# Kernel tuning notes

Measured on AMD Instinct MI355X. Metric: run time of the kernel, lower is better.

Reference implementation:

```python
import jax, jax.numpy as jnp
import numpy as np

IMG = 640
STRIDES = (8, 16, 32)
NUM_CLASSES = 80
TOPK = 10
A_ALPHA = 0.5
A_BETA = 6.0
EPS = 1e-7
CLS_W = 1.0
BOX_W = 2.5


def _make_anchors():
    anchors, strides = [], []
    for s in STRIDES:
        n = IMG // s
        gy, gx = np.meshgrid(np.arange(n, dtype=np.float32), np.arange(n, dtype=np.float32), indexing='ij')
        anchors.append(np.stack([(gx.ravel() + 0.5) * s, (gy.ravel() + 0.5) * s], -1))
        strides.append(np.full((n * n,), s, dtype=np.float32))
    return jnp.asarray(np.concatenate(anchors, 0)), jnp.asarray(np.concatenate(strides, 0))


def _cxcywh_to_xyxy(b):
    cx, cy, w, h = b[..., 0], b[..., 1], b[..., 2], b[..., 3]
    return jnp.stack([cx - w / 2, cy - h / 2, cx + w / 2, cy + h / 2], -1)


def _decode(pred_boxes, anchors, strides):
    # pred_boxes: (B, A, 4) ltrb distances; anchors (A,2); strides (A,)
    d = jax.nn.relu(pred_boxes) * strides[None, :, None]
    x1 = anchors[None, :, 0] - d[..., 0]
    y1 = anchors[None, :, 1] - d[..., 1]
    x2 = anchors[None, :, 0] + d[..., 2]
    y2 = anchors[None, :, 1] + d[..., 3]
    return jnp.stack([x1, y1, x2, y2], -1)


def _box_iou_vs_gt(boxes, gt):
    # boxes: (B, A, 4) xyxy, gt: (B, 4) xyxy -> (B, A)
    lt = jnp.maximum(boxes[..., :2], gt[:, None, :2])
    rb = jnp.minimum(boxes[..., 2:], gt[:, None, 2:])
    wh = jnp.clip(rb - lt, 0.0)
    inter = wh[..., 0] * wh[..., 1]
    a1 = (boxes[..., 2] - boxes[..., 0]) * (boxes[..., 3] - boxes[..., 1])
    a2 = (gt[:, 2] - gt[:, 0]) * (gt[:, 3] - gt[:, 1])
    return inter / (a1 + a2[:, None] - inter)


def _assign(pred_scores, pred_bboxes, anchors, gt_labels, gt_xyxy):
    # Vectorized TaskAlignedAssigner for exactly one gt box per image.
    B, A, C = pred_scores.shape
    cx, cy = anchors[:, 0][None], anchors[:, 1][None]  # (1, A)
    gx1, gy1, gx2, gy2 = (gt_xyxy[:, i:i + 1] for i in range(4))  # (B, 1)
    gt_valid = ((gx2 > gx1) & (gy2 > gy1))[:, 0]  # (B,)
    inside = (cx >= gx1) & (cx <= gx2) & (cy >= gy1) & (cy <= gy2)  # (B, A)
    dist = (cx - (gx1 + gx2) / 2) ** 2 + (cy - (gy1 + gy2) / 2) ** 2
    fallback = jax.nn.one_hot(jnp.argmin(dist, 1), A, dtype=bool)  # nearest anchor if none inside
    mask = jnp.where(inside.any(1, keepdims=True), inside, fallback)
    ious = jnp.clip(_box_iou_vs_gt(pred_bboxes, gt_xyxy), 1e-9)
    cls_s = jax.nn.sigmoid(jnp.take_along_axis(pred_scores, gt_labels[:, None, None], 2)[..., 0])  # (B, A)
    metric = jnp.where(mask, cls_s ** A_ALPHA * ious ** A_BETA, -jnp.inf)
    top_m, top_i = jax.lax.top_k(metric, TOPK)  # (B, TOPK)
    keep = jnp.isfinite(top_m) & gt_valid[:, None]  # handles variable k = min(topk, n_valid) and degenerate gts
    bidx = jnp.arange(B)[:, None]
    fg = jnp.zeros((B, A), bool).at[bidx, top_i].max(keep)
    top_iou = jnp.take_along_axis(ious, top_i, 1)
    tscores = jnp.zeros((B, A, C), pred_scores.dtype).at[bidx, top_i, gt_labels[:, None]].max(jnp.where(keep, top_iou, 0.0))
    tboxes = jnp.where(fg[..., None], gt_xyxy[:, None, :], 0.0)
    return tboxes, tscores, fg


def _focal_sum(logits, targets, alpha=0.25, gamma=2.0):
    p = jax.nn.sigmoid(logits)
    ce = jnp.maximum(logits, 0.0) - logits * targets + jnp.log1p(jnp.exp(-jnp.abs(logits)))
    pt = p * targets + (1 - p) * (1 - targets)
    at = alpha * targets + (1 - alpha) * (1 - targets)
    return jnp.sum(at * ce * (1 - pt) ** gamma)


def _ciou(b1, b2):
    b1x1, b1y1, b1x2, b1y2 = b1[..., 0], b1[..., 1], b1[..., 2], b1[..., 3]
    b2x1, b2y1, b2x2, b2y2 = b2[..., 0], b2[..., 1], b2[..., 2], b2[..., 3]
    w1, h1 = b1x2 - b1x1, b1y2 - b1y1
    w2, h2 = b2x2 - b2x1, b2y2 - b2y1
    inter = jnp.clip(jnp.minimum(b1x2, b2x2) - jnp.maximum(b1x1, b2x1), 0.0) * jnp.clip(jnp.minimum(b1y2, b2y2) - jnp.maximum(b1y1, b2y1), 0.0)
    union = w1 * h1 + w2 * h2 - inter + EPS
    iou = inter / union
    cw = jnp.maximum(b1x2, b2x2) - jnp.minimum(b1x1, b2x1)
    ch = jnp.maximum(b1y2, b2y2) - jnp.minimum(b1y1, b2y1)
    c2 = cw ** 2 + ch ** 2 + EPS
    rho2 = ((b2x1 + b2x2 - b1x1 - b1x2) ** 2 + (b2y1 + b2y2 - b1y1 - b1y2) ** 2) / 4
    v = (4 / jnp.pi ** 2) * (jnp.arctan(w2 / (h2 + EPS)) - jnp.arctan(w1 / (h1 + EPS))) ** 2
    alpha = jax.lax.stop_gradient(v / (v - iou + (1 + EPS)))
    return 1 - iou + rho2 / c2 + alpha * v


def _loss(pred_boxes, pred_scores, gt_bboxes, gt_labels):
    anchors, strides = _make_anchors()
    gt_xyxy = _cxcywh_to_xyxy(gt_bboxes)  # (B, 4)
    pred_xyxy = _decode(pred_boxes, anchors, strides)  # (B, A, 4)
    tboxes, tscores, fg = jax.lax.stop_gradient(
        _assign(pred_scores, pred_xyxy, anchors, gt_labels, gt_xyxy))
    loss_cls = _focal_sum(pred_scores, tscores)
    # mask instead of boolean-index: use pred box as dummy target where not fg (loss masked to 0)
    safe_t = jax.lax.stop_gradient(jnp.where(fg[..., None], tboxes, pred_xyxy))
    loss_box = jnp.sum(_ciou(pred_xyxy, safe_t) * fg.astype(pred_xyxy.dtype))
    npos = jnp.maximum(fg.sum().astype(pred_scores.dtype), 1.0)
    return (loss_cls / npos) * CLS_W + (loss_box / npos) * BOX_W


def setup_inputs() -> dict:
    key = jax.random.key(0)
    k1, k2, k3, k4, k5 = jax.random.split(key, 5)
    B, A, C = 64, 8400, NUM_CLASSES
    pred_boxes = jax.random.normal(k1, (B, A, 4), jnp.float32) + 1.0
    pred_scores = jax.random.normal(k2, (B, A, C), jnp.float32)
    cxcy = jax.random.uniform(k3, (B, 2), jnp.float32, 120.0, 520.0)
    wh = jax.random.uniform(k4, (B, 2), jnp.float32, 60.0, 220.0)
    gt_bboxes = jnp.concatenate([cxcy, wh], -1)  # valid cxcywh boxes inside 640x640
    gt_labels = jax.random.randint(k5, (B,), 0, C)
    return {"pred_boxes": pred_boxes, "pred_scores": pred_scores, "gt_bboxes": gt_bboxes, "gt_labels": gt_labels}


def reference(pred_boxes, pred_scores, gt_bboxes, gt_labels):
    return _loss(pred_boxes, pred_scores, gt_bboxes, gt_labels)
```

## Files before the change

kernel.cpp:

```cpp
#include <hip/hip_runtime.h>
#include <math.h>

#define NCLS 80
#define A_TOT 8400
#define TOPK 10
#define NB_A 64
#define NB_F 448
#define BLK 1024
#define CAND_CAP 1536


__device__ __forceinline__ void anchor_of(int a, float& cx, float& cy, float& st) {
    if (a < 6400)      { int r = a / 80;          int c = a - r * 80;          cx = (c + 0.5f) * 8.0f;  cy = (r + 0.5f) * 8.0f;  st = 8.0f;  }
    else if (a < 8000) { int i = a - 6400; int r = i / 40; int c = i - r * 40; cx = (c + 0.5f) * 16.0f; cy = (r + 0.5f) * 16.0f; st = 16.0f; }
    else               { int i = a - 8000; int r = i / 20; int c = i - r * 20; cx = (c + 0.5f) * 32.0f; cy = (r + 0.5f) * 32.0f; st = 32.0f; }
}

__device__ __forceinline__ float focal0(float l) {
    float e  = __expf(-fabsf(l));
    float ce = fmaxf(l, 0.0f) + __logf(1.0f + e);
    float r  = 1.0f / (1.0f + e);
    float p  = (l >= 0.0f) ? r : e * r;
    return 0.75f * ce * p * p;
}

__device__ __forceinline__ float focal_t(float l, float t) {
    float e  = __expf(-fabsf(l));
    float ce = fmaxf(l, 0.0f) - l * t + __logf(1.0f + e);
    float r  = 1.0f / (1.0f + e);
    float p  = (l >= 0.0f) ? r : e * r;
    float pt = p * t + (1.0f - p) * (1.0f - t);
    float at = 0.75f - 0.5f * t;
    float om = 1.0f - pt;
    return at * ce * om * om;
}

__device__ __forceinline__ float ciou_(float b1x1, float b1y1, float b1x2, float b1y2,
                                       float b2x1, float b2y1, float b2x2, float b2y2) {
    const float EPS = 1e-7f;
    float w1 = b1x2 - b1x1, h1 = b1y2 - b1y1;
    float w2 = b2x2 - b2x1, h2 = b2y2 - b2y1;
    float iw = fmaxf(fminf(b1x2, b2x2) - fmaxf(b1x1, b2x1), 0.0f);
    float ih = fmaxf(fminf(b1y2, b2y2) - fmaxf(b1y1, b2y1), 0.0f);
    float inter = iw * ih;
    float uni = w1 * h1 + w2 * h2 - inter + EPS;
    float iou = inter / uni;
    float cw = fmaxf(b1x2, b2x2) - fminf(b1x1, b2x1);
    float ch = fmaxf(b1y2, b2y2) - fminf(b1y1, b2y1);
    float c2 = cw * cw + ch * ch + EPS;
    float dx = b2x1 + b2x2 - b1x1 - b1x2;
    float dy = b2y1 + b2y2 - b1y1 - b1y2;
    float rho2 = (dx * dx + dy * dy) * 0.25f;
    const float k = 4.0f / (float)(M_PI * M_PI);
    float dv = atanf(w2 / (h2 + EPS)) - atanf(w1 / (h1 + EPS));
    float v = k * dv * dv;
    float alpha = v / (v - iou + 1.0f + EPS);
    return 1.0f - iou + rho2 / c2 + alpha * v;
}


__global__ __launch_bounds__(BLK) void fused_kernel(const float* __restrict__ pred_boxes,
                                                    const float* __restrict__ pred_scores,
                                                    const float* __restrict__ gt_bboxes,
                                                    const int* __restrict__ gt_labels,
                                                    float* __restrict__ ws_focal,
                                                    float* __restrict__ ws_corr,
                                                    float* __restrict__ ws_box,
                                                    int*   __restrict__ ws_np,
                                                    int n4) {
    const int tid = threadIdx.x;

    __shared__ float s_rv[16];
    __shared__ int   s_ri[16];

    if (blockIdx.x >= NB_A) {
        const int fb = blockIdx.x - NB_A;
        float acc = 0.0f;
        const float4* p = (const float4*)pred_scores;
        for (int i = fb * BLK + tid; i < n4; i += NB_F * BLK) {
            float4 v = p[i];
            acc += focal0(v.x) + focal0(v.y) + focal0(v.z) + focal0(v.w);
        }
        for (int o = 32; o > 0; o >>= 1) acc += __shfl_down(acc, o, 64);
        if ((tid & 63) == 0) s_rv[tid >> 6] = acc;
        __syncthreads();
        if (tid < 16) {
            float v = s_rv[tid];
            for (int o = 8; o > 0; o >>= 1) v += __shfl_down(v, o, 64);
            if (tid == 0) ws_focal[fb] = v;
        }
        return;
    }

    const int b = blockIdx.x;

    __shared__ int   s_cnt;
    __shared__ float s_cm[CAND_CAP];
    __shared__ int   s_ci[CAND_CAP];
    __shared__ int   t_idx[TOPK];
    __shared__ float t_val[TOPK];
    __shared__ float s_corr[TOPK], s_boxl[TOPK];
    __shared__ int   s_keep[TOPK];

    const float gcx = gt_bboxes[b * 4 + 0], gcy = gt_bboxes[b * 4 + 1];
    const float gw  = gt_bboxes[b * 4 + 2], gh  = gt_bboxes[b * 4 + 3];
    const float gx1 = gcx - 0.5f * gw, gy1 = gcy - 0.5f * gh;
    const float gx2 = gcx + 0.5f * gw, gy2 = gcy + 0.5f * gh;
    const int   lb  = gt_labels[b];
    const bool  gt_valid = (gx2 > gx1) && (gy2 > gy1);
    const float garea = (gx2 - gx1) * (gy2 - gy1);
    const float gmx = 0.5f * (gx1 + gx2), gmy = 0.5f * (gy1 + gy2);

    if (tid == 0) s_cnt = 0;
    __syncthreads();

    float bestd = INFINITY;
    int   besti = 0x7fffffff;

    for (int a = tid; a < A_TOT; a += BLK) {
        float cx, cy, st;
        anchor_of(a, cx, cy, st);
        float4 pb = ((const float4*)pred_boxes)[b * A_TOT + a];
        float x1 = cx - fmaxf(pb.x, 0.0f) * st;
        float y1 = cy - fmaxf(pb.y, 0.0f) * st;
        float x2 = cx + fmaxf(pb.z, 0.0f) * st;
        float y2 = cy + fmaxf(pb.w, 0.0f) * st;
        bool inside = (cx >= gx1) && (cx <= gx2) && (cy >= gy1) && (cy <= gy2);
        if (inside) {
            float iw = fmaxf(fminf(x2, gx2) - fmaxf(x1, gx1), 0.0f);
            float ih = fmaxf(fminf(y2, gy2) - fmaxf(y1, gy1), 0.0f);
            float inter = iw * ih;
            float iou = fmaxf(inter / ((x2 - x1) * (y2 - y1) + garea - inter), 1e-9f);
            float sc = pred_scores[(size_t)(b * A_TOT + a) * NCLS + lb];
            float cls_s = 1.0f / (1.0f + __expf(-sc));
            float i2 = iou * iou;
            float m = sqrtf(cls_s) * i2 * i2 * i2;
            int pos = atomicAdd(&s_cnt, 1);
            if (pos < CAND_CAP) { s_cm[pos] = m; s_ci[pos] = a; }
        }
        float ddx = cx - gmx, ddy = cy - gmy;
        float d = ddx * ddx + ddy * ddy;
        if (d < bestd) { bestd = d; besti = a; }
    }
    __syncthreads();
    int cnt = min(s_cnt, CAND_CAP);

    if (cnt == 0) {
        float v = bestd; int i = besti;
        for (int o = 32; o > 0; o >>= 1) {
            float ov = __shfl_down(v, o, 64); int oi = __shfl_down(i, o, 64);
            if (ov < v || (ov == v && oi < i)) { v = ov; i = oi; }
        }
        if ((tid & 63) == 0) { s_rv[tid >> 6] = v; s_ri[tid >> 6] = i; }
        __syncthreads();
        if (tid < 16) {
            v = s_rv[tid]; i = s_ri[tid];
            for (int o = 8; o > 0; o >>= 1) {
                float ov = __shfl_down(v, o, 64); int oi = __shfl_down(i, o, 64);
                if (ov < v || (ov == v && oi < i)) { v = ov; i = oi; }
            }
            if (tid == 0) {
                int a = i;
                float cx, cy, st;
                anchor_of(a, cx, cy, st);
                float4 pb = ((const float4*)pred_boxes)[b * A_TOT + a];
                float x1 = cx - fmaxf(pb.x, 0.0f) * st;
                float y1 = cy - fmaxf(pb.y, 0.0f) * st;
                float x2 = cx + fmaxf(pb.z, 0.0f) * st;
                float y2 = cy + fmaxf(pb.w, 0.0f) * st;
                float iw = fmaxf(fminf(x2, gx2) - fmaxf(x1, gx1), 0.0f);
                float ih = fmaxf(fminf(y2, gy2) - fmaxf(y1, gy1), 0.0f);
                float inter = iw * ih;
                float iou = fmaxf(inter / ((x2 - x1) * (y2 - y1) + garea - inter), 1e-9f);
                float sc = pred_scores[(size_t)(b * A_TOT + a) * NCLS + lb];
                float cls_s = 1.0f / (1.0f + __expf(-sc));
                float i2 = iou * iou;
                s_cm[0] = sqrtf(cls_s) * i2 * i2 * i2;
                s_ci[0] = a;
            }
        }
        __syncthreads();
        cnt = 1;
    }

    for (int k = 0; k < TOPK; k++) {
        float v = -INFINITY; int i = 0x7fffffff;
        for (int p = tid; p < cnt; p += BLK) {
            float m = s_cm[p]; int a = s_ci[p];
            if (m > v || (m == v && a < i)) { v = m; i = a; }
        }
        for (int o = 32; o > 0; o >>= 1) {
            float ov = __shfl_down(v, o, 64); int oi = __shfl_down(i, o, 64);
            if (ov > v || (ov == v && oi < i)) { v = ov; i = oi; }
        }
        if ((tid & 63) == 0) { s_rv[tid >> 6] = v; s_ri[tid >> 6] = i; }
        __syncthreads();
        if (tid < 16) {
            v = s_rv[tid]; i = s_ri[tid];
            for (int o = 8; o > 0; o >>= 1) {
                float ov = __shfl_down(v, o, 64); int oi = __shfl_down(i, o, 64);
                if (ov > v || (ov == v && oi < i)) { v = ov; i = oi; }
            }
            if (tid == 0) { t_val[k] = v; t_idx[k] = i; }
        }
        __syncthreads();
        int wa = t_idx[k];
        if (t_val[k] > -INFINITY) {
            for (int p = tid; p < cnt; p += BLK)
                if (s_ci[p] == wa) s_cm[p] = -INFINITY;
        }
        __syncthreads();
    }

    if (tid < TOPK) {
        int   a = t_idx[tid];
        float v = t_val[tid];
        int keep = (v > -INFINITY) && gt_valid;
        float corr = 0.0f, boxl = 0.0f;
        if (keep) {
            float cx, cy, st;
            anchor_of(a, cx, cy, st);
            float4 pb = ((const float4*)pred_boxes)[b * A_TOT + a];
            float x1 = cx - fmaxf(pb.x, 0.0f) * st;
            float y1 = cy - fmaxf(pb.y, 0.0f) * st;
            float x2 = cx + fmaxf(pb.z, 0.0f) * st;
            float y2 = cy + fmaxf(pb.w, 0.0f) * st;
            float iw = fmaxf(fminf(x2, gx2) - fmaxf(x1, gx1), 0.0f);
            float ih = fmaxf(fminf(y2, gy2) - fmaxf(y1, gy1), 0.0f);
            float inter = iw * ih;
            float t = fmaxf(inter / ((x2 - x1) * (y2 - y1) + garea - inter), 1e-9f);
            float l = pred_scores[(size_t)(b * A_TOT + a) * NCLS + lb];
            corr = focal_t(l, t) - focal0(l);
            boxl = ciou_(x1, y1, x2, y2, gx1, gy1, gx2, gy2);
        }
        s_corr[tid] = corr;
        s_boxl[tid] = boxl;
        s_keep[tid] = keep;
    }
    __syncthreads();
    if (tid == 0) {
        float cs = 0.0f, bs = 0.0f;
        int np = 0;
        for (int k = 0; k < TOPK; k++) { cs += s_corr[k]; bs += s_boxl[k]; np += s_keep[k]; }
        ws_corr[b] = cs;
        ws_box[b]  = bs;
        ws_np[b]   = np;
    }
}


__global__ __launch_bounds__(64) void finalize_kernel(const float* __restrict__ ws_focal,
                                                      const float* __restrict__ ws_corr,
                                                      const float* __restrict__ ws_box,
                                                      const int* __restrict__ ws_np,
                                                      float* __restrict__ out, int B) {
    int tid = threadIdx.x;
    float c = 0.0f, bx = 0.0f;
    int np = 0;
    for (int i = tid; i < NB_F; i += 64) c += ws_focal[i];
    for (int i = tid; i < B; i += 64) { c += ws_corr[i]; bx += ws_box[i]; np += ws_np[i]; }
    for (int o = 32; o > 0; o >>= 1) {
        c  += __shfl_down(c, o, 64);
        bx += __shfl_down(bx, o, 64);
        np += __shfl_down(np, o, 64);
    }
    if (tid == 0) {
        float npos = fmaxf((float)np, 1.0f);
        out[0] = c / npos + 2.5f * bx / npos;
    }
}


extern "C" void kernel_launch(void* const* d_in, const int* in_sizes, int n_in,
                              void* d_out, int out_size, void* d_ws, size_t ws_size,
                              hipStream_t stream) {
    const float* pred_boxes  = (const float*)d_in[0];
    const float* pred_scores = (const float*)d_in[1];
    const float* gt_bboxes   = (const float*)d_in[2];
    const int*   gt_labels   = (const int*)d_in[3];
    float* out = (float*)d_out;

    const int B  = in_sizes[3];
    const int n4 = in_sizes[1] / 4;

    float* ws_focal = (float*)d_ws;
    float* ws_corr  = ws_focal + NB_F;
    float* ws_box   = ws_corr + B;
    int*   ws_np    = (int*)(ws_box + B);

    fused_kernel<<<NB_A + NB_F, BLK, 0, stream>>>(pred_boxes, pred_scores, gt_bboxes, gt_labels,
                                                  ws_focal, ws_corr, ws_box, ws_np, n4);
    finalize_kernel<<<1, 64, 0, stream>>>(ws_focal, ws_corr, ws_box, ws_np, out, B);
}
```

Measured before the change: 251.4 us.

## Use dynamic chunk scheduling for focal pass and fuse finalize via last-block reduction

All 512 blocks now take part in the dense focal sum, which pulls chunks of pred_scores from a global atomic counter. The 64 assignment blocks join the pool once their per-image top-k work finishes, so that work is balanced against the bandwidth-bound streaming. The separate finalize kernel is replaced by a last-block-done reduction inside the fused kernel, with workspace entries padded to cache lines. A small init kernel is added to reset the counters, and the chunk loop adds an atomic plus extra barriers per chunk.

After: 278.6 us. 10.8% more time.

```diff
diff --git a/kernel.cpp b/kernel.cpp
--- a/kernel.cpp
+++ b/kernel.cpp
@@ -5,9 +5,12 @@
 #define A_TOT 8400
 #define TOPK 10
 #define NB_A 64
-#define NB_F 448
+#define NBLK 512
 #define BLK 1024
 #define CAND_CAP 1536
+#define FITER 4
+#define CHUNK (BLK * FITER)
+#define LINE 32
 
 
 __device__ __forceinline__ void anchor_of(int a, float& cx, float& cy, float& st) {
@@ -59,41 +62,26 @@
 }
 
 
+__global__ __launch_bounds__(64) void init_kernel(int* __restrict__ counters) {
+    if (threadIdx.x < 2) counters[threadIdx.x] = 0;
+}
+
+
 __global__ __launch_bounds__(BLK) void fused_kernel(const float* __restrict__ pred_boxes,
                                                     const float* __restrict__ pred_scores,
                                                     const float* __restrict__ gt_bboxes,
                                                     const int* __restrict__ gt_labels,
+                                                    int*   __restrict__ counters,
                                                     float* __restrict__ ws_focal,
-                                                    float* __restrict__ ws_corr,
-                                                    float* __restrict__ ws_box,
-                                                    int*   __restrict__ ws_np,
-                                                    int n4) {
+                                                    float* __restrict__ ws_img,
+                                                    float* __restrict__ out,
+                                                    int n4, int B) {
     const int tid = threadIdx.x;
 
     __shared__ float s_rv[16];
     __shared__ int   s_ri[16];
-
-    if (blockIdx.x >= NB_A) {
-        const int fb = blockIdx.x - NB_A;
-        float acc = 0.0f;
-        const float4* p = (const float4*)pred_scores;
-        for (int i = fb * BLK + tid; i < n4; i += NB_F * BLK) {
-            float4 v = p[i];
-            acc += focal0(v.x) + focal0(v.y) + focal0(v.z) + focal0(v.w);
-        }
-        for (int o = 32; o > 0; o >>= 1) acc += __shfl_down(acc, o, 64);
-        if ((tid & 63) == 0) s_rv[tid >> 6] = acc;
-        __syncthreads();
-        if (tid < 16) {
-            float v = s_rv[tid];
-            for (int o = 8; o > 0; o >>= 1) v += __shfl_down(v, o, 64);
-            if (tid == 0) ws_focal[fb] = v;
-        }
-        return;
-    }
-
-    const int b = blockIdx.x;
-
+    __shared__ int   s_chunk;
+    __shared__ int   s_last;
     __shared__ int   s_cnt;
     __shared__ float s_cm[CAND_CAP];
     __shared__ int   s_ci[CAND_CAP];
@@ -102,65 +90,125 @@
     __shared__ float s_corr[TOPK], s_boxl[TOPK];
     __shared__ int   s_keep[TOPK];
 
-    const float gcx = gt_bboxes[b * 4 + 0], gcy = gt_bboxes[b * 4 + 1];
-    const float gw  = gt_bboxes[b * 4 + 2], gh  = gt_bboxes[b * 4 + 3];
-    const float gx1 = gcx - 0.5f * gw, gy1 = gcy - 0.5f * gh;
-    const float gx2 = gcx + 0.5f * gw, gy2 = gcy + 0.5f * gh;
-    const int   lb  = gt_labels[b];
-    const bool  gt_valid = (gx2 > gx1) && (gy2 > gy1);
-    const float garea = (gx2 - gx1) * (gy2 - gy1);
-    const float gmx = 0.5f * (gx1 + gx2), gmy = 0.5f * (gy1 + gy2);
-
-    if (tid == 0) s_cnt = 0;
-    __syncthreads();
-
-    float bestd = INFINITY;
-    int   besti = 0x7fffffff;
-
-    for (int a = tid; a < A_TOT; a += BLK) {
-        float cx, cy, st;
-        anchor_of(a, cx, cy, st);
-        float4 pb = ((const float4*)pred_boxes)[b * A_TOT + a];
-        float x1 = cx - fmaxf(pb.x, 0.0f) * st;
-        float y1 = cy - fmaxf(pb.y, 0.0f) * st;
-        float x2 = cx + fmaxf(pb.z, 0.0f) * st;
-        float y2 = cy + fmaxf(pb.w, 0.0f) * st;
-        bool inside = (cx >= gx1) && (cx <= gx2) && (cy >= gy1) && (cy <= gy2);
-        if (inside) {
-            float iw = fmaxf(fminf(x2, gx2) - fmaxf(x1, gx1), 0.0f);
-            float ih = fmaxf(fminf(y2, gy2) - fmaxf(y1, gy1), 0.0f);
-            float inter = iw * ih;
-            float iou = fmaxf(inter / ((x2 - x1) * (y2 - y1) + garea - inter), 1e-9f);
-            float sc = pred_scores[(size_t)(b * A_TOT + a) * NCLS + lb];
-            float cls_s = 1.0f / (1.0f + __expf(-sc));
-            float i2 = iou * iou;
-            float m = sqrtf(cls_s) * i2 * i2 * i2;
-            int pos = atomicAdd(&s_cnt, 1);
-            if (pos < CAND_CAP) { s_cm[pos] = m; s_ci[pos] = a; }
-        }
-        float ddx = cx - gmx, ddy = cy - gmy;
-        float d = ddx * ddx + ddy * ddy;
-        if (d < bestd) { bestd = d; besti = a; }
-    }
-    __syncthreads();
-    int cnt = min(s_cnt, CAND_CAP);
-
-    if (cnt == 0) {
-        float v = bestd; int i = besti;
-        for (int o = 32; o > 0; o >>= 1) {
-            float ov = __shfl_down(v, o, 64); int oi = __shfl_down(i, o, 64);
-            if (ov < v || (ov == v && oi < i)) { v = ov; i = oi; }
-        }
-        if ((tid & 63) == 0) { s_rv[tid >> 6] = v; s_ri[tid >> 6] = i; }
-        __syncthreads();
-        if (tid < 16) {
-            v = s_rv[tid]; i = s_ri[tid];
-            for (int o = 8; o > 0; o >>= 1) {
+    if (blockIdx.x < NB_A) {
+        const int b = blockIdx.x;
+
+        const float gcx = gt_bboxes[b * 4 + 0], gcy = gt_bboxes[b * 4 + 1];
+        const float gw  = gt_bboxes[b * 4 + 2], gh  = gt_bboxes[b * 4 + 3];
+        const float gx1 = gcx - 0.5f * gw, gy1 = gcy - 0.5f * gh;
+        const float gx2 = gcx + 0.5f * gw, gy2 = gcy + 0.5f * gh;
+        const int   lb  = gt_labels[b];
+        const bool  gt_valid = (gx2 > gx1) && (gy2 > gy1);
+        const float garea = (gx2 - gx1) * (gy2 - gy1);
+        const float gmx = 0.5f * (gx1 + gx2), gmy = 0.5f * (gy1 + gy2);
+
+        if (tid == 0) s_cnt = 0;
+        __syncthreads();
+
+        float bestd = INFINITY;
+        int   besti = 0x7fffffff;
+
+        for (int a = tid; a < A_TOT; a += BLK) {
+            float cx, cy, st;
+            anchor_of(a, cx, cy, st);
+            float4 pb = ((const float4*)pred_boxes)[b * A_TOT + a];
+            float x1 = cx - fmaxf(pb.x, 0.0f) * st;
+            float y1 = cy - fmaxf(pb.y, 0.0f) * st;
+            float x2 = cx + fmaxf(pb.z, 0.0f) * st;
+            float y2 = cy + fmaxf(pb.w, 0.0f) * st;
+            bool inside = (cx >= gx1) && (cx <= gx2) && (cy >= gy1) && (cy <= gy2);
+            if (inside) {
+                float iw = fmaxf(fminf(x2, gx2) - fmaxf(x1, gx1), 0.0f);
+                float ih = fmaxf(fminf(y2, gy2) - fmaxf(y1, gy1), 0.0f);
+                float inter = iw * ih;
+                float iou = fmaxf(inter / ((x2 - x1) * (y2 - y1) + garea - inter), 1e-9f);
+                float sc = pred_scores[(size_t)(b * A_TOT + a) * NCLS + lb];
+                float cls_s = 1.0f / (1.0f + __expf(-sc));
+                float i2 = iou * iou;
+                float m = sqrtf(cls_s) * i2 * i2 * i2;
+                int pos = atomicAdd(&s_cnt, 1);
+                if (pos < CAND_CAP) { s_cm[pos] = m; s_ci[pos] = a; }
+            }
+            float ddx = cx - gmx, ddy = cy - gmy;
+            float d = ddx * ddx + ddy * ddy;
+            if (d < bestd) { bestd = d; besti = a; }
+        }
+        __syncthreads();
+        int cnt = min(s_cnt, CAND_CAP);
+
+        if (cnt == 0) {
+            float v = bestd; int i = besti;
+            for (int o = 32; o > 0; o >>= 1) {
                 float ov = __shfl_down(v, o, 64); int oi = __shfl_down(i, o, 64);
                 if (ov < v || (ov == v && oi < i)) { v = ov; i = oi; }
             }
-            if (tid == 0) {
-                int a = i;
+            if ((tid & 63) == 0) { s_rv[tid >> 6] = v; s_ri[tid >> 6] = i; }
+            __syncthreads();
+            if (tid < 16) {
+                v = s_rv[tid]; i = s_ri[tid];
+                for (int o = 8; o > 0; o >>= 1) {
+                    float ov = __shfl_down(v, o, 64); int oi = __shfl_down(i, o, 64);
+                    if (ov < v || (ov == v && oi < i)) { v = ov; i = oi; }
+                }
+                if (tid == 0) {
+                    int a = i;
+                    float cx, cy, st;
+                    anchor_of(a, cx, cy, st);
+                    float4 pb = ((const float4*)pred_boxes)[b * A_TOT + a];
+                    float x1 = cx - fmaxf(pb.x, 0.0f) * st;
+                    float y1 = cy - fmaxf(pb.y, 0.0f) * st;
+                    float x2 = cx + fmaxf(pb.z, 0.0f) * st;
+                    float y2 = cy + fmaxf(pb.w, 0.0f) * st;
+                    float iw = fmaxf(fminf(x2, gx2) - fmaxf(x1, gx1), 0.0f);
+                    float ih = fmaxf(fminf(y2, gy2) - fmaxf(y1, gy1), 0.0f);
+                    float inter = iw * ih;
+                    float iou = fmaxf(inter / ((x2 - x1) * (y2 - y1) + garea - inter), 1e-9f);
+                    float sc = pred_scores[(size_t)(b * A_TOT + a) * NCLS + lb];
+                    float cls_s = 1.0f / (1.0f + __expf(-sc));
+                    float i2 = iou * iou;
+                    s_cm[0] = sqrtf(cls_s) * i2 * i2 * i2;
+                    s_ci[0] = a;
+                }
+            }
+            __syncthreads();
+            cnt = 1;
+        }
+
+        for (int k = 0; k < TOPK; k++) {
+            float v = -INFINITY; int i = 0x7fffffff;
+            for (int p = tid; p < cnt; p += BLK) {
+                float m = s_cm[p]; int a = s_ci[p];
+                if (m > v || (m == v && a < i)) { v = m; i = a; }
+            }
+            for (int o = 32; o > 0; o >>= 1) {
+                float ov = __shfl_down(v, o, 64); int oi = __shfl_down(i, o, 64);
+                if (ov > v || (ov == v && oi < i)) { v = ov; i = oi; }
+            }
+            if ((tid & 63) == 0) { s_rv[tid >> 6] = v; s_ri[tid >> 6] = i; }
+            __syncthreads();
+            if (tid < 16) {
+                v = s_rv[tid]; i = s_ri[tid];
+                for (int o = 8; o > 0; o >>= 1) {
+                    float ov = __shfl_down(v, o, 64); int oi = __shfl_down(i, o, 64);
+                    if (ov > v || (ov == v && oi < i)) { v = ov; i = oi; }
+                }
+                if (tid == 0) { t_val[k] = v; t_idx[k] = i; }
+            }
+            __syncthreads();
+            int wa = t_idx[k];
+            if (t_val[k] > -INFINITY) {
+                for (int p = tid; p < cnt; p += BLK)
+                    if (s_ci[p] == wa) s_cm[p] = -INFINITY;
+            }
+            __syncthreads();
+        }
+
+        if (tid < TOPK) {
+            int   a = t_idx[tid];
+            float v = t_val[tid];
+            int keep = (v > -INFINITY) && gt_valid;
+            float corr = 0.0f, boxl = 0.0f;
+            if (keep) {
                 float cx, cy, st;
                 anchor_of(a, cx, cy, st);
                 float4 pb = ((const float4*)pred_boxes)[b * A_TOT + a];
@@ -171,102 +219,81 @@
                 float iw = fmaxf(fminf(x2, gx2) - fmaxf(x1, gx1), 0.0f);
                 float ih = fmaxf(fminf(y2, gy2) - fmaxf(y1, gy1), 0.0f);
                 float inter = iw * ih;
-                float iou = fmaxf(inter / ((x2 - x1) * (y2 - y1) + garea - inter), 1e-9f);
-                float sc = pred_scores[(size_t)(b * A_TOT + a) * NCLS + lb];
-                float cls_s = 1.0f / (1.0f + __expf(-sc));
-                float i2 = iou * iou;
-                s_cm[0] = sqrtf(cls_s) * i2 * i2 * i2;
-                s_ci[0] = a;
-            }
-        }
-        __syncthreads();
-        cnt = 1;
+                float t = fmaxf(inter / ((x2 - x1) * (y2 - y1) + garea - inter), 1e-9f);
+                float l = pred_scores[(size_t)(b * A_TOT + a) * NCLS + lb];
+                corr = focal_t(l, t) - focal0(l);
+                boxl = ciou_(x1, y1, x2, y2, gx1, gy1, gx2, gy2);
+            }
+            s_corr[tid] = corr;
+            s_boxl[tid] = boxl;
+            s_keep[tid] = keep;
+        }
+        __syncthreads();
+        if (tid == 0) {
+            float cs = 0.0f, bs = 0.0f;
+            int np = 0;
+            for (int k = 0; k < TOPK; k++) { cs += s_corr[k]; bs += s_boxl[k]; np += s_keep[k]; }
+            float* L = ws_img + b * LINE;
+            L[0] = cs;
+            L[1] = bs;
+            L[2] = (float)np;
+        }
     }
 
-    for (int k = 0; k < TOPK; k++) {
-        float v = -INFINITY; int i = 0x7fffffff;
-        for (int p = tid; p < cnt; p += BLK) {
-            float m = s_cm[p]; int a = s_ci[p];
-            if (m > v || (m == v && a < i)) { v = m; i = a; }
-        }
-        for (int o = 32; o > 0; o >>= 1) {
-            float ov = __shfl_down(v, o, 64); int oi = __shfl_down(i, o, 64);
-            if (ov > v || (ov == v && oi < i)) { v = ov; i = oi; }
-        }
-        if ((tid & 63) == 0) { s_rv[tid >> 6] = v; s_ri[tid >> 6] = i; }
-        __syncthreads();
-        if (tid < 16) {
-            v = s_rv[tid]; i = s_ri[tid];
-            for (int o = 8; o > 0; o >>= 1) {
-                float ov = __shfl_down(v, o, 64); int oi = __shfl_down(i, o, 64);
-                if (ov > v || (ov == v && oi < i)) { v = ov; i = oi; }
-            }
-            if (tid == 0) { t_val[k] = v; t_idx[k] = i; }
-        }
-        __syncthreads();
-        int wa = t_idx[k];
-        if (t_val[k] > -INFINITY) {
-            for (int p = tid; p < cnt; p += BLK)
-                if (s_ci[p] == wa) s_cm[p] = -INFINITY;
-        }
-        __syncthreads();
+    float acc = 0.0f;
+    const float4* p4 = (const float4*)pred_scores;
+    if (tid == 0) s_chunk = atomicAdd(&counters[0], 1);
+    for (;;) {
+        __syncthreads();
+        const int c = s_chunk;
+        const int base = c * CHUNK;
+        if (base >= n4) break;
+        __syncthreads();
+        if (tid == 0) s_chunk = atomicAdd(&counters[0], 1);
+        #pragma unroll
+        for (int k = 0; k < FITER; k++) {
+            int i = base + k * BLK + tid;
+            if (i < n4) {
+                float4 v = p4[i];
+                acc += focal0(v.x) + focal0(v.y) + focal0(v.z) + focal0(v.w);
+            }
+        }
     }
 
-    if (tid < TOPK) {
-        int   a = t_idx[tid];
-        float v = t_val[tid];
-        int keep = (v > -INFINITY) && gt_valid;
-        float corr = 0.0f, boxl = 0.0f;
-        if (keep) {
-            float cx, cy, st;
-            anchor_of(a, cx, cy, st);
-            float4 pb = ((const float4*)pred_boxes)[b * A_TOT + a];
-            float x1 = cx - fmaxf(pb.x, 0.0f) * st;
-            float y1 = cy - fmaxf(pb.y, 0.0f) * st;
-            float x2 = cx + fmaxf(pb.z, 0.0f) * st;
-            float y2 = cy + fmaxf(pb.w, 0.0f) * st;
-            float iw = fmaxf(fminf(x2, gx2) - fmaxf(x1, gx1), 0.0f);
-            float ih = fmaxf(fminf(y2, gy2) - fmaxf(y1, gy1), 0.0f);
-            float inter = iw * ih;
-            float t = fmaxf(inter / ((x2 - x1) * (y2 - y1) + garea - inter), 1e-9f);
-            float l = pred_scores[(size_t)(b * A_TOT + a) * NCLS + lb];
-            corr = focal_t(l, t) - focal0(l);
-            boxl = ciou_(x1, y1, x2, y2, gx1, gy1, gx2, gy2);
-        }
-        s_corr[tid] = corr;
-        s_boxl[tid] = boxl;
-        s_keep[tid] = keep;
+    for (int o = 32; o > 0; o >>= 1) acc += __shfl_down(acc, o, 64);
+    if ((tid & 63) == 0) s_rv[tid >> 6] = acc;
+    __syncthreads();
+    if (tid == 0) {
+        float v = 0.0f;
+        #pragma unroll
+        for (int w = 0; w < BLK / 64; w++) v += s_rv[w];
+        ws_focal[blockIdx.x * LINE] = v;
+        __threadfence();
+        int old = atomicAdd(&counters[1], 1);
+        s_last = (old == NBLK - 1);
     }
     __syncthreads();
-    if (tid == 0) {
-        float cs = 0.0f, bs = 0.0f;
-        int np = 0;
-        for (int k = 0; k < TOPK; k++) { cs += s_corr[k]; bs += s_boxl[k]; np += s_keep[k]; }
-        ws_corr[b] = cs;
-        ws_box[b]  = bs;
-        ws_np[b]   = np;
-    }
-}
-
-
-__global__ __launch_bounds__(64) void finalize_kernel(const float* __restrict__ ws_focal,
-                                                      const float* __restrict__ ws_corr,
-                                                      const float* __restrict__ ws_box,
-                                                      const int* __restrict__ ws_np,
-                                                      float* __restrict__ out, int B) {
-    int tid = threadIdx.x;
-    float c = 0.0f, bx = 0.0f;
-    int np = 0;
-    for (int i = tid; i < NB_F; i += 64) c += ws_focal[i];
-    for (int i = tid; i < B; i += 64) { c += ws_corr[i]; bx += ws_box[i]; np += ws_np[i]; }
-    for (int o = 32; o > 0; o >>= 1) {
-        c  += __shfl_down(c, o, 64);
-        bx += __shfl_down(bx, o, 64);
-        np += __shfl_down(np, o, 64);
-    }
-    if (tid == 0) {
-        float npos = fmaxf((float)np, 1.0f);
-        out[0] = c / npos + 2.5f * bx / npos;
+
+    if (s_last) {
+        __threadfence();
+        if (tid < 64) {
+            float c = 0.0f, bx = 0.0f, np = 0.0f;
+            for (int i = tid; i < NBLK; i += 64)
+                c += ((volatile float*)ws_focal)[i * LINE];
+            for (int i = tid; i < B; i += 64) {
+                volatile float* L = (volatile float*)(ws_img + i * LINE);
+                c += L[0]; bx += L[1]; np += L[2];
+            }
+            for (int o = 32; o > 0; o >>= 1) {
+                c  += __shfl_down(c, o, 64);
+                bx += __shfl_down(bx, o, 64);
+                np += __shfl_down(np, o, 64);
+            }
+            if (tid == 0) {
+                float npos = fmaxf(np, 1.0f);
+                out[0] = c / npos + 2.5f * bx / npos;
+            }
+        }
     }
 }
 
@@ -283,12 +310,11 @@
     const int B  = in_sizes[3];
     const int n4 = in_sizes[1] / 4;
 
-    float* ws_focal = (float*)d_ws;
-    float* ws_corr  = ws_focal + NB_F;
-    float* ws_box   = ws_corr + B;
-    int*   ws_np    = (int*)(ws_box + B);
-
-    fused_kernel<<<NB_A + NB_F, BLK, 0, stream>>>(pred_boxes, pred_scores, gt_bboxes, gt_labels,
-                                                  ws_focal, ws_corr, ws_box, ws_np, n4);
-    finalize_kernel<<<1, 64, 0, stream>>>(ws_focal, ws_corr, ws_box, ws_np, out, B);
-}
+    int*   counters = (int*)d_ws;
+    float* ws_focal = (float*)d_ws + LINE;
+    float* ws_img   = ws_focal + NBLK * LINE;
+
+    init_kernel<<<1, 64, 0, stream>>>(counters);
+    fused_kernel<<<NBLK, BLK, 0, stream>>>(pred_boxes, pred_scores, gt_bboxes, gt_labels,
+                                           counters, ws_focal, ws_img, out, n4, B);
+}
```

## Balance focal-sum work across assign blocks and use fast reciprocal

Applied to the files above, without the earlier changes.

Assignment blocks now also take a share of the dense background focal-loss sum after finishing their per-image work. The work is split into units: each focal block handles two units per stride and each assign block handles one. Focal blocks also issue two independent float4 loads per iteration. The exact division in the focal helpers becomes a hardware reciprocal with one Newton refinement step. The aim is to use the assign blocks' spare capacity and cut ALU cost, at the price of a larger workspace and slightly different rounding.

Result: no change. 248.5 us (-1.1%).

```diff
diff --git a/kernel.cpp b/kernel.cpp
--- a/kernel.cpp
+++ b/kernel.cpp
@@ -8,6 +8,8 @@
 #define NB_F 448
 #define BLK 1024
 #define CAND_CAP 1536
+#define NB_TOT (NB_A + NB_F)
+#define N_UNIT (2 * NB_F + NB_A)
 
 
 __device__ __forceinline__ void anchor_of(int a, float& cx, float& cy, float& st) {
@@ -16,10 +18,15 @@
     else               { int i = a - 8000; int r = i / 20; int c = i - r * 20; cx = (c + 0.5f) * 32.0f; cy = (r + 0.5f) * 32.0f; st = 32.0f; }
 }
 
+__device__ __forceinline__ float rcp_nr(float x) {
+    float r = __builtin_amdgcn_rcpf(x);
+    return r * (2.0f - x * r);
+}
+
 __device__ __forceinline__ float focal0(float l) {
     float e  = __expf(-fabsf(l));
     float ce = fmaxf(l, 0.0f) + __logf(1.0f + e);
-    float r  = 1.0f / (1.0f + e);
+    float r  = rcp_nr(1.0f + e);
     float p  = (l >= 0.0f) ? r : e * r;
     return 0.75f * ce * p * p;
 }
@@ -27,7 +34,7 @@
 __device__ __forceinline__ float focal_t(float l, float t) {
     float e  = __expf(-fabsf(l));
     float ce = fmaxf(l, 0.0f) - l * t + __logf(1.0f + e);
-    float r  = 1.0f / (1.0f + e);
+    float r  = rcp_nr(1.0f + e);
     float p  = (l >= 0.0f) ? r : e * r;
     float pt = p * t + (1.0f - p) * (1.0f - t);
     float at = 0.75f - 0.5f * t;
@@ -73,13 +80,20 @@
     __shared__ float s_rv[16];
     __shared__ int   s_ri[16];
 
+    float acc = 0.0f;
+    const float4* p4 = (const float4*)pred_scores;
+
     if (blockIdx.x >= NB_A) {
         const int fb = blockIdx.x - NB_A;
-        float acc = 0.0f;
-        const float4* p = (const float4*)pred_scores;
-        for (int i = fb * BLK + tid; i < n4; i += NB_F * BLK) {
-            float4 v = p[i];
+        const int base = (2 * fb) * BLK + tid;
+        for (int i = base; i < n4; i += N_UNIT * BLK) {
+            float4 v = p4[i];
             acc += focal0(v.x) + focal0(v.y) + focal0(v.z) + focal0(v.w);
+            int j = i + BLK;
+            if (j < n4) {
+                float4 w = p4[j];
+                acc += focal0(w.x) + focal0(w.y) + focal0(w.z) + focal0(w.w);
+            }
         }
         for (int o = 32; o > 0; o >>= 1) acc += __shfl_down(acc, o, 64);
         if ((tid & 63) == 0) s_rv[tid >> 6] = acc;
@@ -87,7 +101,7 @@
         if (tid < 16) {
             float v = s_rv[tid];
             for (int o = 8; o > 0; o >>= 1) v += __shfl_down(v, o, 64);
-            if (tid == 0) ws_focal[fb] = v;
+            if (tid == 0) ws_focal[blockIdx.x] = v;
         }
         return;
     }
@@ -246,6 +260,22 @@
         ws_box[b]  = bs;
         ws_np[b]   = np;
     }
+
+    {
+        const int base = (2 * NB_F + b) * BLK + tid;
+        for (int i = base; i < n4; i += N_UNIT * BLK) {
+            float4 v = p4[i];
+            acc += focal0(v.x) + focal0(v.y) + focal0(v.z) + focal0(v.w);
+        }
+        for (int o = 32; o > 0; o >>= 1) acc += __shfl_down(acc, o, 64);
+        if ((tid & 63) == 0) s_rv[tid >> 6] = acc;
+        __syncthreads();
+        if (tid < 16) {
+            float v = s_rv[tid];
+            for (int o = 8; o > 0; o >>= 1) v += __shfl_down(v, o, 64);
+            if (tid == 0) ws_focal[blockIdx.x] = v;
+        }
+    }
 }
 
 
@@ -257,7 +287,7 @@
     int tid = threadIdx.x;
     float c = 0.0f, bx = 0.0f;
     int np = 0;
-    for (int i = tid; i < NB_F; i += 64) c += ws_focal[i];
+    for (int i = tid; i < NB_TOT; i += 64) c += ws_focal[i];
     for (int i = tid; i < B; i += 64) { c += ws_corr[i]; bx += ws_box[i]; np += ws_np[i]; }
     for (int o = 32; o > 0; o >>= 1) {
         c  += __shfl_down(c, o, 64);
@@ -284,11 +314,11 @@
     const int n4 = in_sizes[1] / 4;
 
     float* ws_focal = (float*)d_ws;
-    float* ws_corr  = ws_focal + NB_F;
+    float* ws_corr  = ws_focal + NB_TOT;
     float* ws_box   = ws_corr + B;
     int*   ws_np    = (int*)(ws_box + B);
 
-    fused_kernel<<<NB_A + NB_F, BLK, 0, stream>>>(pred_boxes, pred_scores, gt_bboxes, gt_labels,
-                                                  ws_focal, ws_corr, ws_box, ws_np, n4);
+    fused_kernel<<<NB_TOT, BLK, 0, stream>>>(pred_boxes, pred_scores, gt_bboxes, gt_labels,
+                                             ws_focal, ws_corr, ws_box, ws_np, n4);
     finalize_kernel<<<1, 64, 0, stream>>>(ws_focal, ws_corr, ws_box, ws_np, out, B);
 }
```

## Shrink blocks, widen focal grid, unroll loads, and cheapen focal math

Applied to the files above, without the earlier changes.

Reduces block size to 256 threads and raises the number of focal-reduction blocks, with each thread loading four float4s per chunk into two accumulators for more memory-level parallelism. The background focal term is rewritten as log2 of 1+exp(l) times a folded constant, with sigmoid computed via a hardware reciprocal plus one Newton step, to remove a fabs, a select and a divide. Warp-level reductions are adjusted for four waves per block. The new focal formula can overflow for large positive logits, and assignment blocks now have fewer threads for their candidate scans.

Result: slower. 258.7 us (+2.9%).

```diff
diff --git a/kernel.cpp b/kernel.cpp
--- a/kernel.cpp
+++ b/kernel.cpp
@@ -4,10 +4,12 @@
 #define NCLS 80
 #define A_TOT 8400
 #define TOPK 10
+#define BLK 256
 #define NB_A 64
-#define NB_F 448
-#define BLK 1024
+#define NB_F 2048
+#define NB_TOT (NB_A + NB_F)
 #define CAND_CAP 1536
+#define CHUNK 1024
 
 
 __device__ __forceinline__ void anchor_of(int a, float& cx, float& cy, float& st) {
@@ -16,18 +18,24 @@
     else               { int i = a - 8000; int r = i / 20; int c = i - r * 20; cx = (c + 0.5f) * 32.0f; cy = (r + 0.5f) * 32.0f; st = 32.0f; }
 }
 
+__device__ __forceinline__ float rcp_nr(float x) {
+    float r0 = __builtin_amdgcn_rcpf(x);
+    return r0 * __builtin_fmaf(-x, r0, 2.0f);
+}
+
 __device__ __forceinline__ float focal0(float l) {
-    float e  = __expf(-fabsf(l));
-    float ce = fmaxf(l, 0.0f) + __logf(1.0f + e);
-    float r  = 1.0f / (1.0f + e);
-    float p  = (l >= 0.0f) ? r : e * r;
-    return 0.75f * ce * p * p;
+    float w = __expf(l);
+    float u = 1.0f + w;
+    float r = rcp_nr(u);
+    float p = w * r;
+    float s = __log2f(u) * 0.51986038542f;
+    return s * (p * p);
 }
 
 __device__ __forceinline__ float focal_t(float l, float t) {
     float e  = __expf(-fabsf(l));
     float ce = fmaxf(l, 0.0f) - l * t + __logf(1.0f + e);
-    float r  = 1.0f / (1.0f + e);
+    float r  = rcp_nr(1.0f + e);
     float p  = (l >= 0.0f) ? r : e * r;
     float pt = p * t + (1.0f - p) * (1.0f - t);
     float at = 0.75f - 0.5f * t;
@@ -58,35 +66,50 @@
     return 1.0f - iou + rho2 / c2 + alpha * v;
 }
 
-
-__global__ __launch_bounds__(BLK) void fused_kernel(const float* __restrict__ pred_boxes,
-                                                    const float* __restrict__ pred_scores,
-                                                    const float* __restrict__ gt_bboxes,
-                                                    const int* __restrict__ gt_labels,
-                                                    float* __restrict__ ws_focal,
-                                                    float* __restrict__ ws_corr,
-                                                    float* __restrict__ ws_box,
-                                                    int*   __restrict__ ws_np,
-                                                    int n4) {
+__device__ __forceinline__ float focal4(const float4& v) {
+    return (focal0(v.x) + focal0(v.y)) + (focal0(v.z) + focal0(v.w));
+}
+
+
+__global__ __launch_bounds__(BLK, 8) void fused_kernel(const float* __restrict__ pred_boxes,
+                                                       const float* __restrict__ pred_scores,
+                                                       const float* __restrict__ gt_bboxes,
+                                                       const int* __restrict__ gt_labels,
+                                                       float* __restrict__ ws_focal,
+                                                       float* __restrict__ ws_corr,
+                                                       float* __restrict__ ws_box,
+                                                       int*   __restrict__ ws_np,
+                                                       int n4) {
     const int tid = threadIdx.x;
 
-    __shared__ float s_rv[16];
-    __shared__ int   s_ri[16];
+    __shared__ float s_rv[4];
+    __shared__ int   s_ri[4];
 
     if (blockIdx.x >= NB_A) {
         const int fb = blockIdx.x - NB_A;
-        float acc = 0.0f;
-        const float4* p = (const float4*)pred_scores;
-        for (int i = fb * BLK + tid; i < n4; i += NB_F * BLK) {
-            float4 v = p[i];
-            acc += focal0(v.x) + focal0(v.y) + focal0(v.z) + focal0(v.w);
-        }
+        const float4* p4 = (const float4*)pred_scores;
+        float a0 = 0.0f, a1 = 0.0f;
+        for (int c = fb; c * CHUNK < n4; c += NB_F) {
+            const int base = c * CHUNK + tid;
+            const int i0 = base, i1 = base + BLK, i2 = base + 2 * BLK, i3 = base + 3 * BLK;
+            const bool h0 = i0 < n4, h1 = i1 < n4, h2 = i2 < n4, h3 = i3 < n4;
+            float4 v0, v1, v2, v3;
+            if (h0) v0 = p4[i0];
+            if (h1) v1 = p4[i1];
+            if (h2) v2 = p4[i2];
+            if (h3) v3 = p4[i3];
+            if (h0) a0 += focal4(v0);
+            if (h1) a1 += focal4(v1);
+            if (h2) a0 += focal4(v2);
+            if (h3) a1 += focal4(v3);
+        }
+        float acc = a0 + a1;
         for (int o = 32; o > 0; o >>= 1) acc += __shfl_down(acc, o, 64);
         if ((tid & 63) == 0) s_rv[tid >> 6] = acc;
         __syncthreads();
-        if (tid < 16) {
-            float v = s_rv[tid];
-            for (int o = 8; o > 0; o >>= 1) v += __shfl_down(v, o, 64);
+        if (tid < 64) {
+            float v = (tid < 4) ? s_rv[tid] : 0.0f;
+            for (int o = 2; o > 0; o >>= 1) v += __shfl_down(v, o, 64);
             if (tid == 0) ws_focal[fb] = v;
         }
         return;
@@ -153,9 +176,10 @@
         }
         if ((tid & 63) == 0) { s_rv[tid >> 6] = v; s_ri[tid >> 6] = i; }
         __syncthreads();
-        if (tid < 16) {
-            v = s_rv[tid]; i = s_ri[tid];
-            for (int o = 8; o > 0; o >>= 1) {
+        if (tid < 64) {
+            if (tid < 4) { v = s_rv[tid]; i = s_ri[tid]; }
+            else         { v = INFINITY;  i = 0x7fffffff; }
+            for (int o = 2; o > 0; o >>= 1) {
                 float ov = __shfl_down(v, o, 64); int oi = __shfl_down(i, o, 64);
                 if (ov < v || (ov == v && oi < i)) { v = ov; i = oi; }
             }
@@ -195,9 +219,10 @@
         }
         if ((tid & 63) == 0) { s_rv[tid >> 6] = v; s_ri[tid >> 6] = i; }
         __syncthreads();
-        if (tid < 16) {
-            v = s_rv[tid]; i = s_ri[tid];
-            for (int o = 8; o > 0; o >>= 1) {
+        if (tid < 64) {
+            if (tid < 4) { v = s_rv[tid]; i = s_ri[tid]; }
+            else         { v = -INFINITY; i = 0x7fffffff; }
+            for (int o = 2; o > 0; o >>= 1) {
                 float ov = __shfl_down(v, o, 64); int oi = __shfl_down(i, o, 64);
                 if (ov > v || (ov == v && oi < i)) { v = ov; i = oi; }
             }
@@ -288,7 +313,7 @@
     float* ws_box   = ws_corr + B;
     int*   ws_np    = (int*)(ws_box + B);
 
-    fused_kernel<<<NB_A + NB_F, BLK, 0, stream>>>(pred_boxes, pred_scores, gt_bboxes, gt_labels,
-                                                  ws_focal, ws_corr, ws_box, ws_np, n4);
+    fused_kernel<<<NB_TOT, BLK, 0, stream>>>(pred_boxes, pred_scores, gt_bboxes, gt_labels,
+                                             ws_focal, ws_corr, ws_box, ws_np, n4);
     finalize_kernel<<<1, 64, 0, stream>>>(ws_focal, ws_corr, ws_box, ws_np, out, B);
 }
```
